# Kernel tuning notes

Hardware: AMD Instinct MI355X
Metric: run time of the kernel (lower is better)

The kernel has to match this reference:

```python
import jax, jax.numpy as jnp
import numpy as np

B, V, D, H, ET = 64, 64, 64, 64, 2  # batch, num_vars, input_dim, hidden, edge_types


def setup_inputs() -> dict:
    key = jax.random.key(0)
    ks = jax.random.split(key, 6)
    adj = np.ones((V, V)) - np.eye(V)
    send, recv = np.where(adj)  # E = V*(V-1) = 4032 edges, row-major order as in torch code
    E = send.shape[0]
    s = 0.05
    return {
        "inputs": jax.random.normal(ks[0], (B, V, D), jnp.float32),
        "edges": jax.random.uniform(ks[1], (B, E, ET), jnp.float32),
        "W1": jax.random.normal(ks[2], (ET, H, 2 * D), jnp.float32) * s,
        "b1": jnp.zeros((ET, H), jnp.float32),
        "W2": jax.random.normal(ks[3], (ET, H, H), jnp.float32) * s,
        "b2": jnp.zeros((ET, H), jnp.float32),
        "send_idx": jnp.asarray(send, jnp.int32),
        "recv_idx": jnp.asarray(recv, jnp.int32),
    }


def reference(inputs, edges, W1, b1, W2, b2, send_idx, recv_idx):
    # gather node features onto edges: [B, E, 2D]
    pre_msg = jnp.concatenate([inputs[:, recv_idx, :], inputs[:, send_idx, :]], axis=-1)
    all_msgs = jnp.zeros((pre_msg.shape[0], pre_msg.shape[1], H), pre_msg.dtype)
    # skip_first_edge_type=True -> start at 1; eval mode -> dropout p=0 (identity)
    for i in range(1, ET):
        msg = jax.nn.relu(jnp.einsum('bef,hf->beh', pre_msg, W1[i]) + b1[i])
        msg = jax.nn.relu(jnp.einsum('beh,oh->beo', msg, W2[i]) + b2[i])
        all_msgs = all_msgs + msg * edges[:, :, i:i + 1]
    # onehot-matmul aggregation == scatter-sum of edge messages into receiver nodes
    agg_msgs = jnp.zeros((inputs.shape[0], V, H), all_msgs.dtype).at[:, recv_idx, :].add(all_msgs)
    return jnp.concatenate([inputs, agg_msgs], axis=-1)  # [B, V, D+H]
```

## Files before the change

### kernel.cpp

```cpp
#include <hip/hip_runtime.h>
#include <hip/hip_bf16.h>

#define NB 64
#define NV 64
#define ND 64
#define NH 64
#define NE 4032
#define OUTW 128

typedef __bf16 bf16_t;
typedef bf16_t bf16x8 __attribute__((ext_vector_type(8)));
typedef float f32x4 __attribute__((ext_vector_type(4)));

__global__ __launch_bounds__(256, 2)
void gnn_fused(const float* __restrict__ inputs,
               const float* __restrict__ edges,
               const float* __restrict__ W1,
               const float* __restrict__ b1,
               const float* __restrict__ W2,
               const float* __restrict__ b2,
               float* __restrict__ out) {
    __shared__ float  Ylds[NV][NH + 1];
    __shared__ bf16_t Zlds[NV][NH + 8];
    __shared__ float  EW[NE];

    const int blk = blockIdx.x;
    const int b = blk >> 3, oct = blk & 7;
    const int tid = threadIdx.x;
    const int lane = tid & 63, wid = tid >> 6;
    const int lr = lane & 15, lg = lane >> 4;

    const float2* e2 = (const float2*)(edges + b * NE * 2);
    #pragma unroll
    for (int i = 0; i < 16; ++i) {
        int e = i * 256 + tid;
        if (e < NE) EW[e] = e2[e].y;
    }

    bf16x8 wb[4][2];
    float base2[4];
    #pragma unroll
    for (int nt = 0; nt < 4; ++nt) {
        base2[nt] = b2[NH + 16 * nt + lr];
        const float* w2row = W2 + (NH + 16 * nt + lr) * NH;
        #pragma unroll
        for (int ks = 0; ks < 2; ++ks) {
            f32x4 v0 = *(const f32x4*)(w2row + 32 * ks + 8 * lg);
            f32x4 v1 = *(const f32x4*)(w2row + 32 * ks + 8 * lg + 4);
            bf16x8 t;
            #pragma unroll
            for (int q = 0; q < 4; ++q) { t[q] = (bf16_t)v0[q]; t[4 + q] = (bf16_t)v1[q]; }
            wb[nt][ks] = t;
        }
    }

    {
        const float* xrow = inputs + (b * NV + 16 * wid + lr) * ND;
        bf16x8 a[2];
        #pragma unroll
        for (int ks = 0; ks < 2; ++ks) {
            f32x4 v0 = *(const f32x4*)(xrow + 32 * ks + 8 * lg);
            f32x4 v1 = *(const f32x4*)(xrow + 32 * ks + 8 * lg + 4);
            bf16x8 t;
            #pragma unroll
            for (int q = 0; q < 4; ++q) { t[q] = (bf16_t)v0[q]; t[4 + q] = (bf16_t)v1[q]; }
            a[ks] = t;
        }

        f32x4 accY[4], accZ[4];
        #pragma unroll
        for (int nt = 0; nt < 4; ++nt) {
            float base = b1[NH + 16 * nt + lr];
            accY[nt] = (f32x4){base, base, base, base};
            accZ[nt] = (f32x4){0.f, 0.f, 0.f, 0.f};
        }
        #pragma unroll
        for (int nt = 0; nt < 4; ++nt) {
            const float* wrow = W1 + (NH + 16 * nt + lr) * (2 * ND);
            #pragma unroll
            for (int ks = 0; ks < 2; ++ks) {
                f32x4 u0 = *(const f32x4*)(wrow + 32 * ks + 8 * lg);
                f32x4 u1 = *(const f32x4*)(wrow + 32 * ks + 8 * lg + 4);
                f32x4 w0 = *(const f32x4*)(wrow + 64 + 32 * ks + 8 * lg);
                f32x4 w1 = *(const f32x4*)(wrow + 64 + 32 * ks + 8 * lg + 4);
                bf16x8 by, bz;
                #pragma unroll
                for (int q = 0; q < 4; ++q) {
                    by[q] = (bf16_t)u0[q]; by[4 + q] = (bf16_t)u1[q];
                    bz[q] = (bf16_t)w0[q]; bz[4 + q] = (bf16_t)w1[q];
                }
                accY[nt] = __builtin_amdgcn_mfma_f32_16x16x32_bf16(a[ks], by, accY[nt], 0, 0, 0);
                accZ[nt] = __builtin_amdgcn_mfma_f32_16x16x32_bf16(a[ks], bz, accZ[nt], 0, 0, 0);
            }
        }
        #pragma unroll
        for (int nt = 0; nt < 4; ++nt) {
            #pragma unroll
            for (int j = 0; j < 4; ++j) {
                int v = 16 * wid + 4 * lg + j;
                Ylds[v][16 * nt + lr] = accY[nt][j];
                Zlds[v][16 * nt + lr] = (bf16_t)accZ[nt][j];
            }
        }
    }
    __syncthreads();

    #pragma unroll
    for (int rr = 0; rr < 2; ++rr) {
        const int r = oct * 8 + wid * 2 + rr;

        f32x4 y[2][2];
        #pragma unroll
        for (int ks = 0; ks < 2; ++ks) {
            y[ks][0] = *(const f32x4*)(&Ylds[r][32 * ks + 8 * lg]);
            y[ks][1] = *(const f32x4*)(&Ylds[r][32 * ks + 8 * lg + 4]);
        }

        float psum[4] = {0.f, 0.f, 0.f, 0.f};

        #pragma unroll
        for (int mt = 0; mt < 4; ++mt) {
            const int m = 16 * mt + lr;
            const int s = (m < r) ? m : (m == 63 ? r : m + 1);

            bf16x8 afr[2];
            #pragma unroll
            for (int ks = 0; ks < 2; ++ks) {
                bf16x8 z = *(const bf16x8*)(&Zlds[s][32 * ks + 8 * lg]);
                bf16x8 t;
                #pragma unroll
                for (int q = 0; q < 8; ++q) {
                    float vv = (float)z[q] + y[ks][q >> 2][q & 3];
                    t[q] = (bf16_t)(vv > 0.f ? vv : 0.f);
                }
                afr[ks] = t;
            }

            float wj[4];
            #pragma unroll
            for (int j = 0; j < 4; ++j) {
                int me = 16 * mt + 4 * lg + j;
                float w = 0.f;
                if (me < 63) {
                    int se = (me < r) ? me : me + 1;
                    w = EW[se * 63 + r - (se < r ? 1 : 0)];
                }
                wj[j] = w;
            }

            #pragma unroll
            for (int nt = 0; nt < 4; ++nt) {
                f32x4 acc = (f32x4){base2[nt], base2[nt], base2[nt], base2[nt]};
                acc = __builtin_amdgcn_mfma_f32_16x16x32_bf16(afr[0], wb[nt][0], acc, 0, 0, 0);
                acc = __builtin_amdgcn_mfma_f32_16x16x32_bf16(afr[1], wb[nt][1], acc, 0, 0, 0);
                float ss = 0.f;
                #pragma unroll
                for (int j = 0; j < 4; ++j) {
                    float v = acc[j];
                    v = v > 0.f ? v : 0.f;
                    ss = fmaf(v, wj[j], ss);
                }
                psum[nt] += ss;
            }
        }

        #pragma unroll
        for (int nt = 0; nt < 4; ++nt) {
            psum[nt] += __shfl_xor(psum[nt], 16);
            psum[nt] += __shfl_xor(psum[nt], 32);
        }

        float* o = out + (b * NV + r) * OUTW;
        o[lane] = inputs[(b * NV + r) * ND + lane];
        float v = (lg == 0) ? psum[0] : (lg == 1) ? psum[1] : (lg == 2) ? psum[2] : psum[3];
        o[ND + lane] = v;
    }
}

extern "C" void kernel_launch(void* const* d_in, const int* in_sizes, int n_in,
                              void* d_out, int out_size, void* d_ws, size_t ws_size,
                              hipStream_t stream) {
    const float* inputs = (const float*)d_in[0];
    const float* edges  = (const float*)d_in[1];
    const float* W1     = (const float*)d_in[2];
    const float* b1     = (const float*)d_in[3];
    const float* W2     = (const float*)d_in[4];
    const float* b2     = (const float*)d_in[5];

    gnn_fused<<<NB * 8, 256, 0, stream>>>(inputs, edges, W1, b1, W2, b2, (float*)d_out);
}
```

Before: 22.48 us.

## Use 512-thread blocks covering 16 receivers and split node projection across wave halves

Halves the grid to 256 blocks of 512 threads, so each block handles 16 receiver nodes instead of 8. The per-batch prologue (edge-weight staging, W2 conversion and the node-level W1 projection) is therefore repeated half as often. Within the prologue the two wave halves split the Y and Z projections instead of each wave computing both. The tradeoff is fewer blocks on a large GPU and launch bounds of one block per CU-slot, which may lower occupancy.

```diff
diff --git a/kernel.cpp b/kernel.cpp
--- a/kernel.cpp
+++ b/kernel.cpp
@@ -12,7 +12,7 @@
 typedef bf16_t bf16x8 __attribute__((ext_vector_type(8)));
 typedef float f32x4 __attribute__((ext_vector_type(4)));
 
-__global__ __launch_bounds__(256, 2)
+__global__ __launch_bounds__(512, 1)
 void gnn_fused(const float* __restrict__ inputs,
                const float* __restrict__ edges,
                const float* __restrict__ W1,
@@ -25,15 +25,15 @@
     __shared__ float  EW[NE];
 
     const int blk = blockIdx.x;
-    const int b = blk >> 3, oct = blk & 7;
+    const int b = blk >> 2, quad = blk & 3;
     const int tid = threadIdx.x;
     const int lane = tid & 63, wid = tid >> 6;
     const int lr = lane & 15, lg = lane >> 4;
 
     const float2* e2 = (const float2*)(edges + b * NE * 2);
     #pragma unroll
-    for (int i = 0; i < 16; ++i) {
-        int e = i * 256 + tid;
+    for (int i = 0; i < 8; ++i) {
+        int e = i * 512 + tid;
         if (e < NE) EW[e] = e2[e].y;
     }
 
@@ -55,7 +55,11 @@
     }
 
     {
-        const float* xrow = inputs + (b * NV + 16 * wid + lr) * ND;
+        const int half = wid >> 2;
+        const int wt = wid & 3;
+        const int hoff = half * ND;
+
+        const float* xrow = inputs + (b * NV + 16 * wt + lr) * ND;
         bf16x8 a[2];
         #pragma unroll
         for (int ks = 0; ks < 2; ++ks) {
@@ -67,39 +71,32 @@
             a[ks] = t;
         }
 
-        f32x4 accY[4], accZ[4];
+        f32x4 acc[4];
         #pragma unroll
         for (int nt = 0; nt < 4; ++nt) {
-            float base = b1[NH + 16 * nt + lr];
-            accY[nt] = (f32x4){base, base, base, base};
-            accZ[nt] = (f32x4){0.f, 0.f, 0.f, 0.f};
+            float base = (half == 0) ? b1[NH + 16 * nt + lr] : 0.f;
+            acc[nt] = (f32x4){base, base, base, base};
         }
         #pragma unroll
         for (int nt = 0; nt < 4; ++nt) {
-            const float* wrow = W1 + (NH + 16 * nt + lr) * (2 * ND);
+            const float* wrow = W1 + (NH + 16 * nt + lr) * (2 * ND) + hoff;
             #pragma unroll
             for (int ks = 0; ks < 2; ++ks) {
                 f32x4 u0 = *(const f32x4*)(wrow + 32 * ks + 8 * lg);
                 f32x4 u1 = *(const f32x4*)(wrow + 32 * ks + 8 * lg + 4);
-                f32x4 w0 = *(const f32x4*)(wrow + 64 + 32 * ks + 8 * lg);
-                f32x4 w1 = *(const f32x4*)(wrow + 64 + 32 * ks + 8 * lg + 4);
-                bf16x8 by, bz;
+                bf16x8 bw;
                 #pragma unroll
-                for (int q = 0; q < 4; ++q) {
-                    by[q] = (bf16_t)u0[q]; by[4 + q] = (bf16_t)u1[q];
-                    bz[q] = (bf16_t)w0[q]; bz[4 + q] = (bf16_t)w1[q];
-                }
-                accY[nt] = __builtin_amdgcn_mfma_f32_16x16x32_bf16(a[ks], by, accY[nt], 0, 0, 0);
-                accZ[nt] = __builtin_amdgcn_mfma_f32_16x16x32_bf16(a[ks], bz, accZ[nt], 0, 0, 0);
+                for (int q = 0; q < 4; ++q) { bw[q] = (bf16_t)u0[q]; bw[4 + q] = (bf16_t)u1[q]; }
+                acc[nt] = __builtin_amdgcn_mfma_f32_16x16x32_bf16(a[ks], bw, acc[nt], 0, 0, 0);
             }
         }
         #pragma unroll
         for (int nt = 0; nt < 4; ++nt) {
             #pragma unroll
             for (int j = 0; j < 4; ++j) {
-                int v = 16 * wid + 4 * lg + j;
-                Ylds[v][16 * nt + lr] = accY[nt][j];
-                Zlds[v][16 * nt + lr] = (bf16_t)accZ[nt][j];
+                int v = 16 * wt + 4 * lg + j;
+                if (half == 0) Ylds[v][16 * nt + lr] = acc[nt][j];
+                else           Zlds[v][16 * nt + lr] = (bf16_t)acc[nt][j];
             }
         }
     }
@@ -107,7 +104,7 @@
 
     #pragma unroll
     for (int rr = 0; rr < 2; ++rr) {
-        const int r = oct * 8 + wid * 2 + rr;
+        const int r = quad * 16 + wid * 2 + rr;
 
         f32x4 y[2][2];
         #pragma unroll
@@ -187,5 +184,5 @@
     const float* W2     = (const float*)d_in[4];
     const float* b2     = (const float*)d_in[5];
 
-    gnn_fused<<<NB * 8, 256, 0, stream>>>(inputs, edges, W1, b1, W2, b2, (float*)d_out);
+    gnn_fused<<<NB * 4, 512, 0, stream>>>(inputs, edges, W1, b1, W2, b2, (float*)d_out);
 }
```

Result: faster. 20.90 us (-7.1%).
